# Performance work log

Measured on AMD Instinct MI355X. Metric: run time of the kernel, lower is better.

The kernel has to match this reference:

```python
import jax, jax.numpy as jnp
import numpy as np

B, NN, HL = 64, 64, 50
IN_DIM, POS_DIM, ATT_DIM = 384, 64, 256
NEWS_DIM = IN_DIM + POS_DIM  # 448


def setup_inputs() -> dict:
    key = jax.random.key(0)
    ks = jax.random.split(key, 8)
    pos_emb = jax.random.uniform(ks[3], (100, POS_DIM), jnp.float32, -0.1, 0.1)
    pos_emb = pos_emb.at[0].set(0.0)  # initialize() zeros row 0
    return {
        "log_vec": jax.random.normal(ks[0], (B, HL, IN_DIM), jnp.float32),
        "log_mask": jax.random.randint(ks[1], (B, HL), 0, 2, jnp.int32),
        "news_vec": jax.random.normal(ks[2], (B, NN, IN_DIM), jnp.float32),
        "pos_emb": pos_emb,
        "W1": jax.random.normal(ks[4], (ATT_DIM, 2 * NEWS_DIM), jnp.float32) * 0.02,
        "b1": jnp.zeros((ATT_DIM,), jnp.float32),
        "W2": jax.random.normal(ks[5], (1, ATT_DIM), jnp.float32) * 0.02,
        "b2": jnp.zeros((1,), jnp.float32),
    }


def reference(log_vec, log_mask, news_vec, pos_emb, W1, b1, W2, b2):
    b, nn_ = news_vec.shape[:2]
    hl = log_mask.shape[1]
    # append position embeddings (row 0 for candidates, rows 1..hl for history)
    nf = jnp.concatenate(
        [news_vec, jnp.broadcast_to(pos_emb[0], (b, nn_, POS_DIM))], axis=-1)   # (B,NN,ND)
    lf = jnp.concatenate(
        [log_vec, jnp.broadcast_to(pos_emb[1:hl + 1], (b, hl, POS_DIM))], axis=-1)  # (B,HL,ND)
    # affine1(cat[news, log]) == news @ Wn^T + log @ Wl^T + b1 (avoids concat)
    Wn, Wl = W1[:, :NEWS_DIM], W1[:, NEWS_DIM:]
    pn = jnp.einsum('bnd,ad->bna', nf, Wn)   # (B,NN,A)
    pl = jnp.einsum('bhd,ad->bha', lf, Wl)   # (B,HL,A)
    h = jnp.tanh(pn[:, :, None, :] + pl[:, None, :, :] + b1)  # (B,NN,HL,A)
    logits = jnp.einsum('bnha,a->bnh', h, W2[0]) + b2[0]      # (B,NN,HL)
    logits = jnp.where(log_mask[:, None, :] == 0, jnp.float32(-1e9), logits)
    attn = jax.nn.softmax(logits, axis=2)
    user_log_vecs = jnp.einsum('bnh,bhd->bnd', attn, lf)      # (B,NN,ND)
    return user_log_vecs, nf
```

## Files before the change

### kernel.cpp

```cpp
#include <hip/hip_runtime.h>
#include <math.h>

typedef unsigned short u16;
typedef unsigned int   u32;

#define B_       64
#define NN_      64
#define HL_      50
#define IN_DIM   384
#define POS_DIM  64
#define ATT_DIM  256
#define NEWS_DIM 448

typedef __attribute__((ext_vector_type(8))) short short8;
typedef __attribute__((ext_vector_type(4))) float f32x4;

#if __has_builtin(__builtin_amdgcn_exp2f)
#define EXP2F(x) __builtin_amdgcn_exp2f(x)
#else
#define EXP2F(x) exp2f(x)
#endif
#if __has_builtin(__builtin_amdgcn_rcpf)
#define RCPF(x) __builtin_amdgcn_rcpf(x)
#else
#define RCPF(x) (1.0f/(x))
#endif

__device__ __forceinline__ u16 f2bf(float f) {
    union { float f; u32 i; } v; v.f = f;
    u32 r = v.i + 0x7fffu + ((v.i >> 16) & 1u);
    return (u16)(r >> 16);
}
__device__ __forceinline__ float bf2f(u16 u) {
    union { u32 i; float f; } v; v.i = ((u32)u) << 16; return v.f;
}
__device__ __forceinline__ uint2 pack4(float4 v) {
    return make_uint2((u32)f2bf(v.x) | ((u32)f2bf(v.y) << 16),
                      (u32)f2bf(v.z) | ((u32)f2bf(v.w) << 16));
}
__device__ __forceinline__ float fast_tanh(float x) {
    float e = EXP2F(x * 2.88539008f);
    return 1.0f - 2.0f * RCPF(1.0f + e);
}

__global__ __launch_bounds__(256) void prep_k(
    const float* __restrict__ W1, const float* __restrict__ newsv,
    const float* __restrict__ logv, const float* __restrict__ pos,
    u16* __restrict__ Wbf, u16* __restrict__ nv_bf, u16* __restrict__ lf_bf,
    float* __restrict__ nf)
{
    u32 bid = blockIdx.x, tid = threadIdx.x;
    if (bid < 2936u) {
        u32 x = bid & 7u, j = bid >> 3;
        if (j < 192u) {
            u32 idx = j * 256u + tid;
            u32 r = 512u * x + idx / 96u, d4 = idx % 96u;
            float4 v = *(const float4*)(newsv + (size_t)r * IN_DIM + d4 * 4u);
            *(uint2*)(nv_bf + (size_t)r * IN_DIM + d4 * 4u) = pack4(v);
            *(float4*)(nf + (size_t)r * NEWS_DIM + d4 * 4u) = v;
        } else if (j < 342u) {
            u32 idx = (j - 192u) * 256u + tid;
            u32 r = 400u * x + idx / 96u, d4 = idx % 96u;
            float4 v = *(const float4*)(logv + (size_t)r * IN_DIM + d4 * 4u);
            *(uint2*)(lf_bf + (size_t)r * NEWS_DIM + d4 * 4u) = pack4(v);
        } else {
            u32 idx = (j - 342u) * 256u + tid;
            u32 r = 400u * x + idx / 16u, d4 = idx % 16u;
            u32 h = r % HL_;
            float4 v = *(const float4*)(pos + (size_t)(1u + h) * POS_DIM + d4 * 4u);
            *(uint2*)(lf_bf + (size_t)r * NEWS_DIM + IN_DIM + d4 * 4u) = pack4(v);
        }
        return;
    }
    bid -= 2936u;
    if (bid < 224u) {
        u32 i = bid * 256u + tid;
        float4 v = *(const float4*)(W1 + (size_t)i * 4u);
        *(uint2*)(Wbf + (size_t)i * 4u) = pack4(v);
        return;
    }
    bid -= 224u;
    {
        u32 i = bid * 256u + tid;
        u32 r = i / 16u, d4 = i % 16u;
        *(float4*)(nf + (size_t)r * NEWS_DIM + IN_DIM + d4 * 4u) =
            make_float4(0.f, 0.f, 0.f, 0.f);
    }
}

__global__ __launch_bounds__(64) void gemm_k(
    const u16* __restrict__ nv_bf, const u16* __restrict__ lf_bf,
    const u16* __restrict__ Wbf, const float* __restrict__ b1,
    float* __restrict__ pn, float* __restrict__ plT)
{
    int bid = blockIdx.x;
    int lane = threadIdx.x;
    int m = lane & 15, q = lane >> 4;
    int x = bid & 7, j = bid >> 3;
    bool is_pn = j < 128;
    int r0, c0, lda, koff, klen;
    const u16* A;
    if (is_pn) {
        int b = x * 8 + (j >> 4);
        r0 = b * 64 + ((j >> 2) & 3) * 16;
        c0 = (j & 3) * 64;
        A = nv_bf; lda = IN_DIM;   koff = 0;        klen = IN_DIM;
    } else {
        int j2 = j - 128;
        r0 = 400 * x + (j2 >> 2) * 16;
        c0 = (j2 & 3) * 64;
        A = lf_bf; lda = NEWS_DIM; koff = NEWS_DIM; klen = NEWS_DIM;
    }

    f32x4 acc[4];
#pragma unroll
    for (int b = 0; b < 4; b++) acc[b] = (f32x4){0.f, 0.f, 0.f, 0.f};

    const u16* Ap = A + (size_t)(r0 + m) * lda + q * 8;
    const u16* Wp = Wbf + (size_t)(c0 + m) * (2 * NEWS_DIM) + koff + q * 8;

    for (int k = 0; k < klen; k += 32) {
        short8 af, wf[4];
        af = *(const short8*)(Ap + k);
#pragma unroll
        for (int ct = 0; ct < 4; ct++) wf[ct] = *(const short8*)(Wp + ct * 16 * (2 * NEWS_DIM) + k);
#pragma unroll
        for (int ct = 0; ct < 4; ct++)
            acc[ct] = __builtin_amdgcn_mfma_f32_16x16x32_bf16(af, wf[ct], acc[ct], 0, 0, 0);
    }
#pragma unroll
    for (int ct = 0; ct < 4; ct++)
#pragma unroll
        for (int i = 0; i < 4; i++) {
            int gr = r0 + q * 4 + i;
            int gc = c0 + ct * 16 + m;
            float v = acc[ct][i];
            if (is_pn) {
                pn[(size_t)gr * ATT_DIM + gc] = v + b1[gc];
            } else {
                int bb = gr / HL_, hh = gr - bb * HL_;
                plT[(size_t)(bb * ATT_DIM + gc) * HL_ + hh] = v;
            }
        }
}

__global__ __launch_bounds__(256) void attn_out_k(
    const float* __restrict__ pn, const float* __restrict__ plT,
    const float* __restrict__ w2, const int* __restrict__ lmask,
    const u16* __restrict__ lf_bf, float* __restrict__ out)
{
    __shared__ float at_s[4][64];
    int lane = threadIdx.x & 63;
    int wid = __builtin_amdgcn_readfirstlane((int)(threadIdx.x >> 6));
    int x     = blockIdx.x & 7;
    int local = blockIdx.x >> 3;
    int b     = x * 8 + (local >> 4);
    int sub   = local & 15;
    int g     = b * 64 + sub * 4 + wid;
    int n_hl  = (lane < HL_) ? lane : (HL_ - 1);
    const float* pr = pn + (size_t)g * ATT_DIM;
    const float* pl = plT + (size_t)b * ATT_DIM * HL_ + n_hl;

    float a0 = 0.f, a1 = 0.f, a2 = 0.f, a3 = 0.f;
#pragma unroll 4
    for (int a = 0; a < ATT_DIM; a += 4) {
        float4 w4 = *(const float4*)(w2 + a);
        float4 p  = *(const float4*)(pr + a);
        float l0 = pl[(a + 0) * HL_];
        float l1 = pl[(a + 1) * HL_];
        float l2 = pl[(a + 2) * HL_];
        float l3 = pl[(a + 3) * HL_];
        a0 = __builtin_fmaf(fast_tanh(p.x + l0), w4.x, a0);
        a1 = __builtin_fmaf(fast_tanh(p.y + l1), w4.y, a1);
        a2 = __builtin_fmaf(fast_tanh(p.z + l2), w4.z, a2);
        a3 = __builtin_fmaf(fast_tanh(p.w + l3), w4.w, a3);
    }
    float acc = (a0 + a1) + (a2 + a3);
    int mv = (lane < HL_) ? lmask[b * HL_ + lane] : 0;
    float logit = mv ? acc : -1e9f;
    float mx = logit;
#pragma unroll
    for (int o = 32; o > 0; o >>= 1) mx = fmaxf(mx, __shfl_xor(mx, o));
    float e = EXP2F((logit - mx) * 1.44269504f);
    float s = e;
#pragma unroll
    for (int o = 32; o > 0; o >>= 1) s += __shfl_xor(s, o);
    at_s[wid][lane] = e * RCPF(s);

    const u32* lfb32 = (const u32*)(lf_bf + (size_t)b * HL_ * NEWS_DIM);
    int tidx = 192 + (lane & 31);
    float p0 = 0.f, p1 = 0.f, p2 = 0.f, p3 = 0.f,
          p4 = 0.f, p5 = 0.f, p6 = 0.f, p7 = 0.f;
    for (int h = 0; h < HL_; h++) {
        float av = at_s[wid][h];
        const u32* r32 = lfb32 + h * (NEWS_DIM / 2);
        u32 v0 = r32[lane];
        u32 v1 = r32[lane + 64];
        u32 v2 = r32[lane + 128];
        u32 v3 = r32[tidx];
        p0 = fmaf(av, bf2f((u16)v0),         p0);
        p1 = fmaf(av, bf2f((u16)(v0 >> 16)), p1);
        p2 = fmaf(av, bf2f((u16)v1),         p2);
        p3 = fmaf(av, bf2f((u16)(v1 >> 16)), p3);
        p4 = fmaf(av, bf2f((u16)v2),         p4);
        p5 = fmaf(av, bf2f((u16)(v2 >> 16)), p5);
        p6 = fmaf(av, bf2f((u16)v3),         p6);
        p7 = fmaf(av, bf2f((u16)(v3 >> 16)), p7);
    }
    float* orow = out + (size_t)g * NEWS_DIM;
    *(float2*)(orow +       2 * lane) = make_float2(p0, p1);
    *(float2*)(orow + 128 + 2 * lane) = make_float2(p2, p3);
    *(float2*)(orow + 256 + 2 * lane) = make_float2(p4, p5);
    if (lane < 32)
        *(float2*)(orow + 384 + 2 * lane) = make_float2(p6, p7);
}

extern "C" void kernel_launch(void* const* d_in, const int* in_sizes, int n_in,
                              void* d_out, int out_size, void* d_ws, size_t ws_size,
                              hipStream_t stream) {
    const float* logv  = (const float*)d_in[0];
    const int*   lmask = (const int*)d_in[1];
    const float* newsv = (const float*)d_in[2];
    const float* pos   = (const float*)d_in[3];
    const float* W1    = (const float*)d_in[4];
    const float* b1    = (const float*)d_in[5];
    const float* w2    = (const float*)d_in[6];

    float* out = (float*)d_out;
    float* nf  = out + (size_t)B_ * NN_ * NEWS_DIM;

    char* ws = (char*)d_ws;
    u16*   lf_bf = (u16*)(ws + 0);
    u16*   Wbf   = (u16*)(ws + 2867200);
    u16*   nv_bf = (u16*)(ws + 3325952);
    float* pn    = (float*)(ws + 6471680);
    float* plT   = (float*)(ws + 10665984);

    prep_k    <<<3416, 256, 0, stream>>>(W1, newsv, logv, pos,
                                         Wbf, nv_bf, lf_bf, nf);
    gemm_k    <<<1824, 64, 0, stream>>>(nv_bf, lf_bf, Wbf, b1, pn, plT);
    attn_out_k<<<1024, 256, 0, stream>>>(pn, plT, w2, lmask, lf_bf, out);
}
```

Measured before the change: 127.7 us.

## Split attention dims across waves and share plT/lf loads across four news rows

```diff
diff --git a/kernel.cpp b/kernel.cpp
--- a/kernel.cpp
+++ b/kernel.cpp
@@ -149,33 +149,63 @@
     const float* __restrict__ w2, const int* __restrict__ lmask,
     const u16* __restrict__ lf_bf, float* __restrict__ out)
 {
-    __shared__ float at_s[4][64];
+    __shared__ float part[4][4][64];
+    __shared__ float at4[64][4];
     int lane = threadIdx.x & 63;
     int wid = __builtin_amdgcn_readfirstlane((int)(threadIdx.x >> 6));
     int x     = blockIdx.x & 7;
     int local = blockIdx.x >> 3;
     int b     = x * 8 + (local >> 4);
-    int sub   = local & 15;
-    int g     = b * 64 + sub * 4 + wid;
+    int n0    = (local & 15) * 4;
+    int g0    = b * 64 + n0;
     int n_hl  = (lane < HL_) ? lane : (HL_ - 1);
-    const float* pr = pn + (size_t)g * ATT_DIM;
-    const float* pl = plT + (size_t)b * ATT_DIM * HL_ + n_hl;
-
-    float a0 = 0.f, a1 = 0.f, a2 = 0.f, a3 = 0.f;
+
+    int a0 = wid * 64;
+    const float* pl  = plT + ((size_t)b * ATT_DIM + a0) * HL_ + n_hl;
+    const float* pr0 = pn + (size_t)(g0 + 0) * ATT_DIM + a0;
+    const float* pr1 = pn + (size_t)(g0 + 1) * ATT_DIM + a0;
+    const float* pr2 = pn + (size_t)(g0 + 2) * ATT_DIM + a0;
+    const float* pr3 = pn + (size_t)(g0 + 3) * ATT_DIM + a0;
+    const float* w2o = w2 + a0;
+
+    float c0 = 0.f, c1 = 0.f, c2 = 0.f, c3 = 0.f;
+    float d0 = 0.f, d1 = 0.f, d2 = 0.f, d3 = 0.f;
 #pragma unroll 4
-    for (int a = 0; a < ATT_DIM; a += 4) {
-        float4 w4 = *(const float4*)(w2 + a);
-        float4 p  = *(const float4*)(pr + a);
+    for (int a = 0; a < 64; a += 4) {
+        float4 w4 = *(const float4*)(w2o + a);
+        float4 pA = *(const float4*)(pr0 + a);
+        float4 pB = *(const float4*)(pr1 + a);
+        float4 pC = *(const float4*)(pr2 + a);
+        float4 pD = *(const float4*)(pr3 + a);
         float l0 = pl[(a + 0) * HL_];
         float l1 = pl[(a + 1) * HL_];
         float l2 = pl[(a + 2) * HL_];
         float l3 = pl[(a + 3) * HL_];
-        a0 = __builtin_fmaf(fast_tanh(p.x + l0), w4.x, a0);
-        a1 = __builtin_fmaf(fast_tanh(p.y + l1), w4.y, a1);
-        a2 = __builtin_fmaf(fast_tanh(p.z + l2), w4.z, a2);
-        a3 = __builtin_fmaf(fast_tanh(p.w + l3), w4.w, a3);
-    }
-    float acc = (a0 + a1) + (a2 + a3);
+        c0 = __builtin_fmaf(fast_tanh(pA.x + l0), w4.x, c0);
+        d0 = __builtin_fmaf(fast_tanh(pA.y + l1), w4.y, d0);
+        c0 = __builtin_fmaf(fast_tanh(pA.z + l2), w4.z, c0);
+        d0 = __builtin_fmaf(fast_tanh(pA.w + l3), w4.w, d0);
+        c1 = __builtin_fmaf(fast_tanh(pB.x + l0), w4.x, c1);
+        d1 = __builtin_fmaf(fast_tanh(pB.y + l1), w4.y, d1);
+        c1 = __builtin_fmaf(fast_tanh(pB.z + l2), w4.z, c1);
+        d1 = __builtin_fmaf(fast_tanh(pB.w + l3), w4.w, d1);
+        c2 = __builtin_fmaf(fast_tanh(pC.x + l0), w4.x, c2);
+        d2 = __builtin_fmaf(fast_tanh(pC.y + l1), w4.y, d2);
+        c2 = __builtin_fmaf(fast_tanh(pC.z + l2), w4.z, c2);
+        d2 = __builtin_fmaf(fast_tanh(pC.w + l3), w4.w, d2);
+        c3 = __builtin_fmaf(fast_tanh(pD.x + l0), w4.x, c3);
+        d3 = __builtin_fmaf(fast_tanh(pD.y + l1), w4.y, d3);
+        c3 = __builtin_fmaf(fast_tanh(pD.z + l2), w4.z, c3);
+        d3 = __builtin_fmaf(fast_tanh(pD.w + l3), w4.w, d3);
+    }
+    part[wid][0][lane] = c0 + d0;
+    part[wid][1][lane] = c1 + d1;
+    part[wid][2][lane] = c2 + d2;
+    part[wid][3][lane] = c3 + d3;
+    __syncthreads();
+
+    float acc = (part[0][wid][lane] + part[1][wid][lane])
+              + (part[2][wid][lane] + part[3][wid][lane]);
     int mv = (lane < HL_) ? lmask[b * HL_ + lane] : 0;
     float logit = mv ? acc : -1e9f;
     float mx = logit;
@@ -185,34 +215,30 @@
     float s = e;
 #pragma unroll
     for (int o = 32; o > 0; o >>= 1) s += __shfl_xor(s, o);
-    at_s[wid][lane] = e * RCPF(s);
-
+    at4[lane][wid] = e * RCPF(s);
+    __syncthreads();
+
+    int l56 = (lane < 56) ? lane : 55;
+    int k   = wid * 56 + l56;
     const u32* lfb32 = (const u32*)(lf_bf + (size_t)b * HL_ * NEWS_DIM);
-    int tidx = 192 + (lane & 31);
-    float p0 = 0.f, p1 = 0.f, p2 = 0.f, p3 = 0.f,
-          p4 = 0.f, p5 = 0.f, p6 = 0.f, p7 = 0.f;
+    float q00 = 0.f, q01 = 0.f, q10 = 0.f, q11 = 0.f;
+    float q20 = 0.f, q21 = 0.f, q30 = 0.f, q31 = 0.f;
     for (int h = 0; h < HL_; h++) {
-        float av = at_s[wid][h];
-        const u32* r32 = lfb32 + h * (NEWS_DIM / 2);
-        u32 v0 = r32[lane];
-        u32 v1 = r32[lane + 64];
-        u32 v2 = r32[lane + 128];
-        u32 v3 = r32[tidx];
-        p0 = fmaf(av, bf2f((u16)v0),         p0);
-        p1 = fmaf(av, bf2f((u16)(v0 >> 16)), p1);
-        p2 = fmaf(av, bf2f((u16)v1),         p2);
-        p3 = fmaf(av, bf2f((u16)(v1 >> 16)), p3);
-        p4 = fmaf(av, bf2f((u16)v2),         p4);
-        p5 = fmaf(av, bf2f((u16)(v2 >> 16)), p5);
-        p6 = fmaf(av, bf2f((u16)v3),         p6);
-        p7 = fmaf(av, bf2f((u16)(v3 >> 16)), p7);
-    }
-    float* orow = out + (size_t)g * NEWS_DIM;
-    *(float2*)(orow +       2 * lane) = make_float2(p0, p1);
-    *(float2*)(orow + 128 + 2 * lane) = make_float2(p2, p3);
-    *(float2*)(orow + 256 + 2 * lane) = make_float2(p4, p5);
-    if (lane < 32)
-        *(float2*)(orow + 384 + 2 * lane) = make_float2(p6, p7);
+        float4 av = *(const float4*)at4[h];
+        u32 v = lfb32[h * (NEWS_DIM / 2) + k];
+        float f0 = bf2f((u16)v), f1 = bf2f((u16)(v >> 16));
+        q00 = fmaf(av.x, f0, q00);  q01 = fmaf(av.x, f1, q01);
+        q10 = fmaf(av.y, f0, q10);  q11 = fmaf(av.y, f1, q11);
+        q20 = fmaf(av.z, f0, q20);  q21 = fmaf(av.z, f1, q21);
+        q30 = fmaf(av.w, f0, q30);  q31 = fmaf(av.w, f1, q31);
+    }
+    if (lane < 56) {
+        float* o0 = out + (size_t)g0 * NEWS_DIM + 2 * k;
+        *(float2*)(o0)                = make_float2(q00, q01);
+        *(float2*)(o0 + NEWS_DIM)     = make_float2(q10, q11);
+        *(float2*)(o0 + 2 * NEWS_DIM) = make_float2(q20, q21);
+        *(float2*)(o0 + 3 * NEWS_DIM) = make_float2(q30, q31);
+    }
 }
 
 extern "C" void kernel_launch(void* const* d_in, const int* in_sizes, int n_in,
```

Result: faster. 124.3 us (-2.7%).
